# Kernel optimization log

Measured on AMD Instinct MI355X. Metric: run time of the kernel, lower is better.

## Reference

```python
import jax, jax.numpy as jnp
import numpy as np
import math

B, C, RES, N, H = 32, 32, 16, 16384, 64
G = RES ** 3
RATIO = 1.0


def _halton2(n):
    # 2-D Halton sequence (radical inverse, bases 2 and 3), shape (2, n)
    def radinv(idx, base):
        inv = np.zeros(n, dtype=np.float64)
        f = 1.0 / base
        i = idx.copy()
        while i.max() > 0:
            inv += f * (i % base)
            i //= base
            f /= base
        return inv
    idx = np.arange(1, n + 1)
    return np.stack([radinv(idx, 2), radinv(idx, 3)], axis=0).astype(np.float32)


def setup_inputs() -> dict:
    key = jax.random.key(0)
    ks = jax.random.split(key, 3)
    rng = np.random.default_rng(0)
    x = jax.random.normal(ks[0], (B, C, RES, RES, RES), dtype=jnp.float32)
    # density-driven counts: per-batch multinomial allocation summing exactly to N
    dens = rng.random((B, G)) ** 2
    probs = dens / dens.sum(axis=1, keepdims=True)
    counts = np.stack([rng.multinomial(N, probs[b]) for b in range(B)]).astype(np.int32)
    # grid offsets: ((meshgrid + 0.5) / res - 0.5).view(3, -1)  (normalize_ratio = 0.5)
    grid = np.stack(np.meshgrid(np.arange(RES), np.arange(RES), np.arange(RES), indexing='ij'), 0).astype(np.float32)
    grid_o = ((grid + 0.5) / RES - 0.5).reshape(3, -1)
    # Halton noise scaled: b_rnd * ratio - ratio/2, broadcast to batch
    b_rnd = _halton2(N) * RATIO - RATIO / 2.0
    b_rnd = np.broadcast_to(b_rnd[None], (B, 2, N)).copy()
    # pointwise generator MLP: (C+2) -> H -> 3
    W1 = jax.random.normal(ks[1], (H, C + 2), dtype=jnp.float32) * 0.05
    b1 = jnp.zeros((H,), dtype=jnp.float32)
    W2 = jax.random.normal(ks[2], (3, H), dtype=jnp.float32) * 0.05
    b2 = jnp.zeros((3,), dtype=jnp.float32)
    return {"x": x, "counts": jnp.asarray(counts), "b_rnd": jnp.asarray(b_rnd),
            "grid_o": jnp.asarray(grid_o), "W1": W1, "b1": b1, "W2": W2, "b2": b2}


def reference(x, counts, b_rnd, grid_o, W1, b1, W2, b2):
    b, c = x.shape[0], x.shape[1]
    n = b_rnd.shape[-1]
    xf = x.reshape(b, c, -1)                      # (b, c, G)
    # repeat_interleave(x[:, ind], counts[ind]) with fixed output size n:
    # output slot j maps to cell idx = searchsorted(cumsum(counts), j, 'right')
    cum = jnp.cumsum(counts, axis=1)              # (b, G)
    slots = jnp.arange(n)
    idx = jax.vmap(lambda cs: jnp.searchsorted(cs, slots, side='right'))(cum)  # (b, n)
    x_ind = jnp.take_along_axis(xf, idx[:, None, :], axis=2)                   # (b, c, n)
    o_ind = jnp.transpose(grid_o[:, idx], (1, 0, 2))                           # (b, 3, n)
    b_inp = jnp.concatenate([x_ind, b_rnd], axis=1)                            # (b, c+2, n)
    h = jax.nn.relu(jnp.einsum('hc,bcn->bhn', W1, b_inp) + b1[None, :, None])
    out = jnp.einsum('oh,bhn->bon', W2, h) + b2[None, :, None]                 # (b, 3, n)
    norm = jnp.linalg.norm(out, axis=1)                                        # (b, n)
    reg = jnp.clip(norm - math.sqrt(3.0) / RES, 0.0)
    return out + o_ind, reg
```

## Files before the change

### kernel.cpp

```cpp
#include <hip/hip_runtime.h>
#include <math.h>

constexpr int B_ = 32;
constexpr int C_ = 32;
constexpr int RES_ = 16;
constexpr int G_ = RES_ * RES_ * RES_;
constexpr int N_ = 16384;
constexpr int H_ = 64;
__device__ constexpr float REG_THR = 0.10825317547305483f;

typedef __attribute__((ext_vector_type(2))) float v2f;

__device__ __forceinline__ v2f fma2(v2f a, v2f b, v2f c) {
    return __builtin_elementwise_fma(a, b, c);
}

__device__ __forceinline__ unsigned short f2bf(float f) {
    union { float f; unsigned int u; } v; v.f = f;
    const unsigned int r = v.u + 0x7FFFu + ((v.u >> 16) & 1u);
    return (unsigned short)(r >> 16);
}

constexpr int TCELL = 128;
constexpr int RS = 33;
constexpr int WROW = 36;

__global__ __launch_bounds__(256) void hx_scan_kernel(
    const float* __restrict__ x, const float* __restrict__ W1,
    const float* __restrict__ b1, const int* __restrict__ counts,
    unsigned short* __restrict__ hxb, int* __restrict__ idxarr) {
    const int b = blockIdx.y;
    const int t = threadIdx.x;

    __shared__ float __align__(16) s_w1[H_ * WROW];
    __shared__ unsigned int s_hx[TCELL * RS];

    if (blockIdx.x == G_ / TCELL) {
        int* partials = (int*)s_w1;
        const int* cb = counts + b * G_;
        const int base = t * 16;
        int local[16];
        int s = 0;
#pragma unroll
        for (int i = 0; i < 16; ++i) { s += cb[base + i]; local[i] = s; }
        partials[t] = s;
        __syncthreads();
        for (int off = 1; off < 256; off <<= 1) {
            int v = (t >= off) ? partials[t - off] : 0;
            __syncthreads();
            partials[t] += v;
            __syncthreads();
        }
        const int prev = (t > 0) ? partials[t - 1] : 0;

        int* ib = idxarr + b * N_;
        int startk = prev;
#pragma unroll
        for (int i = 0; i < 16; ++i) {
            const int endk = prev + local[i];
            const int cell = base + i;
            const int k0 = startk > 0 ? startk : 0;
            const int k1 = endk < N_ ? endk : N_;
            for (int k = k0; k < k1; ++k) ib[k] = cell;
            startk = endk;
        }
        return;
    }

    const int tile = blockIdx.x * TCELL;
    const int cell_l = t & 63;
    const int hh2 = __builtin_amdgcn_readfirstlane((t >> 6) * 8);

    for (int i = t; i < H_ * 34; i += 256) {
        const int r = i / 34;
        const int c = i - r * 34;
        s_w1[r * WROW + c] = W1[i];
    }
    if (t < H_) s_w1[t * WROW + 34] = b1[t];

    const float* xb = x + ((size_t)b * C_) * G_ + tile + cell_l;
    v2f xv0[C_ / 2], xv1[C_ / 2];
#pragma unroll
    for (int c2 = 0; c2 < C_ / 2; ++c2) {
        xv0[c2].x = xb[(size_t)(2 * c2 + 0) * G_];
        xv0[c2].y = xb[(size_t)(2 * c2 + 1) * G_];
        xv1[c2].x = xb[(size_t)(2 * c2 + 0) * G_ + 64];
        xv1[c2].y = xb[(size_t)(2 * c2 + 1) * G_ + 64];
    }
    __syncthreads();

    unsigned int* row0 = s_hx + cell_l * RS + hh2;
    unsigned int* row1 = s_hx + (cell_l + 64) * RS + hh2;
#pragma unroll 2
    for (int j = 0; j < 8; ++j) {
        const float* we = s_w1 + (2 * (hh2 + j) + 0) * WROW;
        const float* wo = s_w1 + (2 * (hh2 + j) + 1) * WROW;
        v2f e0p = {0.f, 0.f}, q0p = {0.f, 0.f};
        v2f e1p = {0.f, 0.f}, q1p = {0.f, 0.f};
#pragma unroll
        for (int c2 = 0; c2 < C_ / 2; ++c2) {
            const v2f wep = *(const v2f*)(we + 2 * c2);
            const v2f wop = *(const v2f*)(wo + 2 * c2);
            e0p = fma2(wep, xv0[c2], e0p);
            q0p = fma2(wop, xv0[c2], q0p);
            e1p = fma2(wep, xv1[c2], e1p);
            q1p = fma2(wop, xv1[c2], q1p);
        }
        const float e0 = we[34] + e0p.x + e0p.y;
        const float q0 = wo[34] + q0p.x + q0p.y;
        const float e1 = we[34] + e1p.x + e1p.y;
        const float q1 = wo[34] + q1p.x + q1p.y;
        row0[j] = (unsigned int)f2bf(e0) | ((unsigned int)f2bf(q0) << 16);
        row1[j] = (unsigned int)f2bf(e1) | ((unsigned int)f2bf(q1) << 16);
    }
    __syncthreads();

    uint4* ob4 = (uint4*)(hxb + ((size_t)b * G_ + tile) * H_);
#pragma unroll
    for (int k = 0; k < 4; ++k) {
        const int L4 = t + k * 256;
        const int cell = L4 >> 3;
        const int base = (L4 & 7) * 4;
        const unsigned int* s = s_hx + cell * RS + base;
        ob4[L4] = make_uint4(s[0], s[1], s[2], s[3]);
    }
}

__global__ __launch_bounds__(256) void point_kernel(
    const unsigned short* __restrict__ hxb, const float* __restrict__ b_rnd,
    const float* __restrict__ W1, const float* __restrict__ W2,
    const float* __restrict__ b2, const int* __restrict__ idxarr,
    float* __restrict__ out0, float* __restrict__ reg_out) {
    const int b = blockIdx.y;
    const int n = blockIdx.x * 256 + threadIdx.x;

    const int idx = idxarr[(size_t)b * N_ + n] & (G_ - 1);
    const float r0 = b_rnd[((size_t)b * 2 + 0) * N_ + n];
    const float r1 = b_rnd[((size_t)b * 2 + 1) * N_ + n];
    const unsigned short* hp = hxb + ((size_t)b * G_ + idx) * H_;

    v2f o0p = {0.f, 0.f}, o1p = {0.f, 0.f}, o2p = {0.f, 0.f};
    const v2f zz = {0.f, 0.f};
#pragma unroll
    for (int g = 0; g < 8; ++g) {
        const uint4 u = *(const uint4*)(hp + g * 8);
        const unsigned int uw[4] = {u.x, u.y, u.z, u.w};
#pragma unroll
        for (int q = 0; q < 4; ++q) {
            const int h = g * 8 + 2 * q;
            union { unsigned int u; float f; } a, bwd;
            a.u = uw[q] << 16;
            bwd.u = uw[q] & 0xFFFF0000u;
            float he = a.f, ho = bwd.f;
            he = fmaf(W1[h * 34 + 32], r0, he);
            he = fmaf(W1[h * 34 + 33], r1, he);
            ho = fmaf(W1[(h + 1) * 34 + 32], r0, ho);
            ho = fmaf(W1[(h + 1) * 34 + 33], r1, ho);
            v2f hv2; hv2.x = he; hv2.y = ho;
            hv2 = __builtin_elementwise_max(hv2, zz);
            o0p = fma2(*(const v2f*)(W2 + 0 * H_ + h), hv2, o0p);
            o1p = fma2(*(const v2f*)(W2 + 1 * H_ + h), hv2, o1p);
            o2p = fma2(*(const v2f*)(W2 + 2 * H_ + h), hv2, o2p);
        }
    }
    float o0 = b2[0] + o0p.x + o0p.y;
    float o1 = b2[1] + o1p.x + o1p.y;
    float o2 = b2[2] + o2p.x + o2p.y;

    const float nrm = sqrtf(o0 * o0 + o1 * o1 + o2 * o2);
    const float reg = fmaxf(nrm - REG_THR, 0.0f);

    o0 += (float)((idx >> 8) & 15) * 0.0625f - 0.46875f;
    o1 += (float)((idx >> 4) & 15) * 0.0625f - 0.46875f;
    o2 += (float)(idx & 15) * 0.0625f - 0.46875f;

    float* p = out0 + ((size_t)b * 3) * N_ + n;
    p[0]              = o0;
    p[N_]             = o1;
    p[2 * (size_t)N_] = o2;
    reg_out[(size_t)b * N_ + n] = reg;
}

extern "C" void kernel_launch(void* const* d_in, const int* in_sizes, int n_in,
                              void* d_out, int out_size, void* d_ws, size_t ws_size,
                              hipStream_t stream) {
    const float* x      = (const float*)d_in[0];
    const int*   counts = (const int*)  d_in[1];
    const float* b_rnd  = (const float*)d_in[2];
    const float* W1     = (const float*)d_in[4];
    const float* b1     = (const float*)d_in[5];
    const float* W2     = (const float*)d_in[6];
    const float* b2     = (const float*)d_in[7];

    float* out  = (float*)d_out;
    float* rout = out + (size_t)B_ * 3 * N_;

    int* idxarr = (int*)d_ws;
    unsigned short* hxb =
        (unsigned short*)((char*)d_ws + (size_t)B_ * N_ * sizeof(int));

    dim3 gridA(G_ / TCELL + 1, B_);
    dim3 gridB(N_ / 256, B_);

    hx_scan_kernel<<<gridA, 256, 0, stream>>>(x, W1, b1, counts, hxb, idxarr);
    point_kernel<<<gridB, 256, 0, stream>>>(hxb, b_rnd, W1, W2, b2,
                                            idxarr, out, rout);
}
```

Measured before the change: 104.7 us.

## Process four cell groups per thread in hx kernel with float4 weight loads

Doubles the cell tile per block so each thread computes hidden projections for four cells instead of two. Each shared-memory weight value is now reused across more cells, and the weights are read as float4 instead of float2. This cuts LDS traffic per FMA, but it roughly doubles the x register footprint (128 floats), which risks lower occupancy or spills, and halves the number of blocks.

```diff
diff --git a/kernel.cpp b/kernel.cpp
--- a/kernel.cpp
+++ b/kernel.cpp
@@ -21,7 +21,7 @@
     return (unsigned short)(r >> 16);
 }
 
-constexpr int TCELL = 128;
+constexpr int TCELL = 256;
 constexpr int RS = 33;
 constexpr int WROW = 36;
 
@@ -79,45 +79,63 @@
     if (t < H_) s_w1[t * WROW + 34] = b1[t];
 
     const float* xb = x + ((size_t)b * C_) * G_ + tile + cell_l;
-    v2f xv0[C_ / 2], xv1[C_ / 2];
+    v2f xv0[C_ / 2], xv1[C_ / 2], xv2[C_ / 2], xv3[C_ / 2];
 #pragma unroll
     for (int c2 = 0; c2 < C_ / 2; ++c2) {
-        xv0[c2].x = xb[(size_t)(2 * c2 + 0) * G_];
-        xv0[c2].y = xb[(size_t)(2 * c2 + 1) * G_];
-        xv1[c2].x = xb[(size_t)(2 * c2 + 0) * G_ + 64];
-        xv1[c2].y = xb[(size_t)(2 * c2 + 1) * G_ + 64];
+        const size_t o0 = (size_t)(2 * c2 + 0) * G_;
+        const size_t o1 = (size_t)(2 * c2 + 1) * G_;
+        xv0[c2].x = xb[o0];       xv0[c2].y = xb[o1];
+        xv1[c2].x = xb[o0 + 64];  xv1[c2].y = xb[o1 + 64];
+        xv2[c2].x = xb[o0 + 128]; xv2[c2].y = xb[o1 + 128];
+        xv3[c2].x = xb[o0 + 192]; xv3[c2].y = xb[o1 + 192];
     }
     __syncthreads();
 
-    unsigned int* row0 = s_hx + cell_l * RS + hh2;
-    unsigned int* row1 = s_hx + (cell_l + 64) * RS + hh2;
+    unsigned int* row0 = s_hx + (cell_l +   0) * RS + hh2;
+    unsigned int* row1 = s_hx + (cell_l +  64) * RS + hh2;
+    unsigned int* row2 = s_hx + (cell_l + 128) * RS + hh2;
+    unsigned int* row3 = s_hx + (cell_l + 192) * RS + hh2;
 #pragma unroll 2
     for (int j = 0; j < 8; ++j) {
         const float* we = s_w1 + (2 * (hh2 + j) + 0) * WROW;
         const float* wo = s_w1 + (2 * (hh2 + j) + 1) * WROW;
         v2f e0p = {0.f, 0.f}, q0p = {0.f, 0.f};
         v2f e1p = {0.f, 0.f}, q1p = {0.f, 0.f};
-#pragma unroll
-        for (int c2 = 0; c2 < C_ / 2; ++c2) {
-            const v2f wep = *(const v2f*)(we + 2 * c2);
-            const v2f wop = *(const v2f*)(wo + 2 * c2);
-            e0p = fma2(wep, xv0[c2], e0p);
-            q0p = fma2(wop, xv0[c2], q0p);
-            e1p = fma2(wep, xv1[c2], e1p);
-            q1p = fma2(wop, xv1[c2], q1p);
-        }
-        const float e0 = we[34] + e0p.x + e0p.y;
-        const float q0 = wo[34] + q0p.x + q0p.y;
-        const float e1 = we[34] + e1p.x + e1p.y;
-        const float q1 = wo[34] + q1p.x + q1p.y;
+        v2f e2p = {0.f, 0.f}, q2p = {0.f, 0.f};
+        v2f e3p = {0.f, 0.f}, q3p = {0.f, 0.f};
+#pragma unroll
+        for (int c4 = 0; c4 < C_ / 4; ++c4) {
+            const float4 we4 = *(const float4*)(we + 4 * c4);
+            const float4 wo4 = *(const float4*)(wo + 4 * c4);
+            v2f wea; wea.x = we4.x; wea.y = we4.y;
+            v2f web; web.x = we4.z; web.y = we4.w;
+            v2f woa; woa.x = wo4.x; woa.y = wo4.y;
+            v2f wob; wob.x = wo4.z; wob.y = wo4.w;
+            const int ca = 2 * c4, cb2 = 2 * c4 + 1;
+            e0p = fma2(wea, xv0[ca], e0p); e0p = fma2(web, xv0[cb2], e0p);
+            q0p = fma2(woa, xv0[ca], q0p); q0p = fma2(wob, xv0[cb2], q0p);
+            e1p = fma2(wea, xv1[ca], e1p); e1p = fma2(web, xv1[cb2], e1p);
+            q1p = fma2(woa, xv1[ca], q1p); q1p = fma2(wob, xv1[cb2], q1p);
+            e2p = fma2(wea, xv2[ca], e2p); e2p = fma2(web, xv2[cb2], e2p);
+            q2p = fma2(woa, xv2[ca], q2p); q2p = fma2(wob, xv2[cb2], q2p);
+            e3p = fma2(wea, xv3[ca], e3p); e3p = fma2(web, xv3[cb2], e3p);
+            q3p = fma2(woa, xv3[ca], q3p); q3p = fma2(wob, xv3[cb2], q3p);
+        }
+        const float be = we[34], bo = wo[34];
+        const float e0 = be + e0p.x + e0p.y, q0 = bo + q0p.x + q0p.y;
+        const float e1 = be + e1p.x + e1p.y, q1 = bo + q1p.x + q1p.y;
+        const float e2 = be + e2p.x + e2p.y, q2 = bo + q2p.x + q2p.y;
+        const float e3 = be + e3p.x + e3p.y, q3 = bo + q3p.x + q3p.y;
         row0[j] = (unsigned int)f2bf(e0) | ((unsigned int)f2bf(q0) << 16);
         row1[j] = (unsigned int)f2bf(e1) | ((unsigned int)f2bf(q1) << 16);
+        row2[j] = (unsigned int)f2bf(e2) | ((unsigned int)f2bf(q2) << 16);
+        row3[j] = (unsigned int)f2bf(e3) | ((unsigned int)f2bf(q3) << 16);
     }
     __syncthreads();
 
     uint4* ob4 = (uint4*)(hxb + ((size_t)b * G_ + tile) * H_);
 #pragma unroll
-    for (int k = 0; k < 4; ++k) {
+    for (int k = 0; k < 8; ++k) {
         const int L4 = t + k * 256;
         const int cell = L4 >> 3;
         const int base = (L4 & 7) * 4;
```

New measurement: 106.5 us. Within noise of the previous version (+1.7%).
